# Kernel optimization log

Measured on AMD Instinct MI355X. Metric: run time of the kernel, lower is better.

## Reference

```python
import jax, jax.numpy as jnp
import numpy as np

N_NODES = 100000
N_EDGES = 1600000
IN_DIM, HID_DIM, OUT_DIM = 128, 256, 512
BN_EPS = 1e-5


def setup_inputs() -> dict:
    key = jax.random.key(0)
    ks = jax.random.split(key, 10)
    x = jax.random.normal(ks[0], (N_NODES, IN_DIM), dtype=jnp.float32)
    edge_index = jax.random.randint(ks[1], (2, N_EDGES), 0, N_NODES, dtype=jnp.int64)
    def lin(k, o, i):
        return jax.random.normal(k, (o, i), dtype=jnp.float32) * (1.0 / np.sqrt(i))
    return {
        "x": x,
        "edge_index": edge_index,
        # SAGEConv 1: in_dim -> hidden_dim (lin_l has bias, lin_r has none)
        "W1l": lin(ks[2], HID_DIM, IN_DIM),
        "b1": jnp.zeros((HID_DIM,), dtype=jnp.float32),
        "W1r": lin(ks[3], HID_DIM, IN_DIM),
        # BatchNorm1d(hidden_dim)
        "gamma": jnp.ones((HID_DIM,), dtype=jnp.float32),
        "beta": jnp.zeros((HID_DIM,), dtype=jnp.float32),
        # SAGEConv 2: hidden_dim -> gnn_out_dim
        "W2l": lin(ks[4], OUT_DIM, HID_DIM),
        "b2": jnp.zeros((OUT_DIM,), dtype=jnp.float32),
        "W2r": lin(ks[5], OUT_DIM, HID_DIM),
    }


def _sage_max(h, src, dst, Wl, b, Wr, n_nodes):
    # gather source features, max-aggregate onto destination nodes
    agg = jax.ops.segment_max(h[src], dst, num_segments=n_nodes)  # [N, D]
    agg = jnp.where(jnp.isneginf(agg), 0.0, agg)  # PyG fills empty segments with 0
    return agg @ Wl.T + b + h @ Wr.T


def reference(x, edge_index, W1l, b1, W1r, gamma, beta, W2l, b2, W2r):
    src, dst = edge_index[0], edge_index[1]
    n = x.shape[0]
    # layer 1: SAGEConv(in_dim, hidden_dim, aggr='max')
    h = _sage_max(x, src, dst, W1l, b1, W1r, n)
    # BatchNorm1d (batch statistics), Dropout is identity in eval; no activation in 'sage' branch
    mean = jnp.mean(h, axis=0)
    var = jnp.var(h, axis=0)
    h = gamma * (h - mean) * jax.lax.rsqrt(var + BN_EPS) + beta
    # layer 2: SAGEConv(hidden_dim, gnn_out_dim, aggr='max')
    out = _sage_max(h, src, dst, W2l, b2, W2r, n)
    return out
```

## Files before the change

kernel.cpp:

```cpp
#include <hip/hip_runtime.h>
#include <hip/hip_bf16.h>
#include <stdint.h>

#define N_NODES 100000
#define N_EDGES 1600000
#define IN_DIM 128
#define HID_DIM 256
#define OUT_DIM 512
#define NBUK 391
#define BCAP 8192
#define EPB 4096

typedef __attribute__((ext_vector_type(4))) float f32x4;
typedef __attribute__((ext_vector_type(8))) short bf16x8;

__device__ __forceinline__ float bf16lo(uint32_t u){ uint32_t b = u << 16; return __builtin_bit_cast(float, b); }
__device__ __forceinline__ float bf16hi(uint32_t u){ uint32_t b = u & 0xffff0000u; return __builtin_bit_cast(float, b); }
__device__ __forceinline__ uint16_t f32_to_bf16(float f){
  uint32_t u = __builtin_bit_cast(uint32_t, f);
  uint32_t r = (u + 0x7fffu + ((u >> 16) & 1u)) >> 16;
  return (uint16_t)r;
}
__device__ __forceinline__ uint32_t pack_bf16_exact(float lo, float hi){
  return (__builtin_bit_cast(uint32_t, hi) & 0xffff0000u) | (__builtin_bit_cast(uint32_t, lo) >> 16);
}
__device__ __forceinline__ uint32_t pack_bf16_rne(float lo, float hi){
  return (uint32_t)f32_to_bf16(lo) | ((uint32_t)f32_to_bf16(hi) << 16);
}
__device__ __forceinline__ void gl2lds16(const void* g, void* l){
  __builtin_amdgcn_global_load_lds(
      (const __attribute__((address_space(1))) uint32_t*)g,
      (__attribute__((address_space(3))) uint32_t*)l, 16, 0, 0);
}

__global__ void k_convx(const float* __restrict__ x, uint16_t* __restrict__ X1x,
                        int* __restrict__ gcur, float* __restrict__ sum,
                        float* __restrict__ sumsq){
  if (blockIdx.x == 12500){
    const int t = threadIdx.x;
    for (int i = t; i < NBUK; i += 256) gcur[i] = i << 13;
    sum[t] = 0.f; sumsq[t] = 0.f;
    return;
  }
  const int idx = blockIdx.x * 256 + threadIdx.x;
  const int n = idx >> 5, q = idx & 31;
  const float4 v = *(const float4*)(x + (long)n * 128 + q * 4);
  ushort4 o;
  o.x = f32_to_bf16(v.x); o.y = f32_to_bf16(v.y);
  o.z = f32_to_bf16(v.z); o.w = f32_to_bf16(v.w);
  *(ushort4*)(X1x + (long)n * 128 + q * 4) = o;
}

__global__ void k_bucket(const int* __restrict__ src, const int* __restrict__ dst,
                         int* __restrict__ gcur, int* __restrict__ ebuk){
  __shared__ int hist[NBUK], curs[NBUK], base[NBUK];
  const int tid = threadIdx.x;
  const int e0 = blockIdx.x * EPB;
  for (int t = tid; t < NBUK; t += 256) hist[t] = 0;
  __syncthreads();
  for (int i = 0; i < EPB; i += 256){
    int e = e0 + i + tid;
    if (e < N_EDGES) atomicAdd(&hist[dst[e] >> 8], 1);
  }
  __syncthreads();
  for (int t = tid; t < NBUK; t += 256){
    int h = hist[t];
    base[t] = h ? atomicAdd(&gcur[t], h) : 0;
    curs[t] = 0;
  }
  __syncthreads();
  for (int i = 0; i < EPB; i += 256){
    int e = e0 + i + tid;
    if (e < N_EDGES){
      int d = dst[e];
      int b = d >> 8;
      int idx = atomicAdd(&curs[b], 1);
      int pos = base[b] + idx;
      if (pos < ((b + 1) << 13))
        ebuk[pos] = ((d & 255) << 17) | src[e];
    }
  }
}

__global__ __launch_bounds__(256)
void k_fillc(const int* __restrict__ gcur, const int* __restrict__ ebuk,
             int* __restrict__ row_start, int* __restrict__ esrc){
  __shared__ int ebuf[BCAP];
  __shared__ int cnt[256];
  __shared__ int wtot[4];
  __shared__ int red[4];
  const int b = blockIdx.x, tid = threadIdx.x, lane = tid & 63, wv = tid >> 6;
  const int nodebase = b << 8;
  const int nodecnt = min(256, N_NODES - nodebase);
  int accb = 0;
  for (int t = tid; t < b; t += 256) accb += gcur[t] - (t << 13);
  #pragma unroll
  for (int d = 32; d > 0; d >>= 1) accb += __shfl_xor(accb, d);
  if (lane == 0) red[wv] = accb;
  int size_b = gcur[b] - (b << 13);
  if (size_b > BCAP) size_b = BCAP;
  cnt[tid] = 0;
  for (int i = tid; i < size_b; i += 256) ebuf[i] = ebuk[(b << 13) + i];
  __syncthreads();
  const int bs = red[0] + red[1] + red[2] + red[3];
  for (int i = tid; i < size_b; i += 256) atomicAdd(&cnt[ebuf[i] >> 17], 1);
  __syncthreads();
  const int c = cnt[tid];
  int v = c;
  #pragma unroll
  for (int d = 1; d < 64; d <<= 1){ int t = __shfl_up(v, d); if (lane >= d) v += t; }
  if (lane == 63) wtot[wv] = v;
  __syncthreads();
  if (tid < 4){
    int t = wtot[tid];
    #pragma unroll
    for (int d = 1; d < 4; d <<= 1){ int u = __shfl_up(t, d); if (tid >= d) t += u; }
    wtot[tid] = t;
  }
  __syncthreads();
  const int excl = (wv ? wtot[wv - 1] : 0) + (v - c);
  if (tid < nodecnt) row_start[nodebase + tid] = bs + excl;
  if (b == NBUK - 1 && tid == 0) row_start[N_NODES] = N_EDGES;
  cnt[tid] = excl;
  __syncthreads();
  for (int i = tid; i < size_b; i += 256){
    int p = ebuf[i];
    int pos = atomicAdd(&cnt[p >> 17], 1);
    esrc[bs + pos] = p & 0x1FFFF;
  }
}

__global__ void k_w1(const float* __restrict__ W1l, const float* __restrict__ W1r,
                     uint16_t* __restrict__ W1cat){
  int idx = blockIdx.x * 256 + threadIdx.x;
  int j = idx >> 8, k = idx & 255;
  float v = (k < 128) ? W1l[j * 128 + k] : W1r[j * 128 + (k - 128)];
  W1cat[idx] = f32_to_bf16(v);
}

__global__ void k_w2(const float* __restrict__ W2l, const float* __restrict__ W2r,
                     const float* __restrict__ b2, const float* __restrict__ sum,
                     const float* __restrict__ sumsq, const float* __restrict__ gamma,
                     const float* __restrict__ beta, uint16_t* __restrict__ W2cat,
                     float* __restrict__ bias2, float* __restrict__ scale_g,
                     float* __restrict__ shift_g){
  __shared__ float sc_s[256], sh_s[256];
  const int tid = threadIdx.x;
  {
    const float inv_n = 1.0f / (float)N_NODES;
    float mean = sum[tid] * inv_n;
    float var = sumsq[tid] * inv_n - mean * mean;
    float sc = gamma[tid] * rsqrtf(var + 1e-5f);
    float sh = beta[tid] - mean * sc;
    sc_s[tid] = sc; sh_s[tid] = sh;
    if (blockIdx.x == 0){ scale_g[tid] = sc; shift_g[tid] = sh; }
  }
  __syncthreads();
  const int wid = (blockIdx.x * 256 + tid) >> 6;
  const int lane = tid & 63;
  float part = 0.f;
  #pragma unroll
  for (int t = 0; t < 4; t++){
    int k = t * 64 + lane;
    float wl = W2l[(long)wid * 256 + k];
    W2cat[(long)wid * 512 + k] = f32_to_bf16(wl);
    float wr = W2r[(long)wid * 256 + k];
    W2cat[(long)wid * 512 + 256 + k] = f32_to_bf16(wr * sc_s[k]);
    part += sh_s[k] * wr;
  }
  #pragma unroll
  for (int d = 32; d > 0; d >>= 1) part += __shfl_xor(part, d);
  if (lane == 0) bias2[wid] = b2[wid] + part;
}

__global__ void k_agg1(const uint32_t* __restrict__ X1x, const int* __restrict__ row_start,
                       const int* __restrict__ esrc, uint32_t* __restrict__ X1agg){
  const int wid = (blockIdx.x * 256 + threadIdx.x) >> 6;
  const int lane = threadIdx.x & 63;
  if (wid >= N_NODES) return;
  const int grp = lane >> 4, li = lane & 15;
  const int s0 = row_start[wid], s1 = row_start[wid + 1];
  float m[8];
  #pragma unroll
  for (int j = 0; j < 8; j++) m[j] = -INFINITY;

  #define ACC1(u)                                        \
    m[0] = fmaxf(m[0], bf16lo(u.x)); m[1] = fmaxf(m[1], bf16hi(u.x)); \
    m[2] = fmaxf(m[2], bf16lo(u.y)); m[3] = fmaxf(m[3], bf16hi(u.y)); \
    m[4] = fmaxf(m[4], bf16lo(u.z)); m[5] = fmaxf(m[5], bf16hi(u.z)); \
    m[6] = fmaxf(m[6], bf16lo(u.w)); m[7] = fmaxf(m[7], bf16hi(u.w));

  int e = s0 + grp;
  for (; e + 12 < s1; e += 16){
    const uint4 ua = *(const uint4*)(X1x + (long)esrc[e] * 64 + li * 4);
    const uint4 ub = *(const uint4*)(X1x + (long)esrc[e + 4] * 64 + li * 4);
    const uint4 uc = *(const uint4*)(X1x + (long)esrc[e + 8] * 64 + li * 4);
    const uint4 ud = *(const uint4*)(X1x + (long)esrc[e + 12] * 64 + li * 4);
    ACC1(ua); ACC1(ub); ACC1(uc); ACC1(ud);
  }
  for (; e < s1; e += 4){
    const uint4 u = *(const uint4*)(X1x + (long)esrc[e] * 64 + li * 4);
    ACC1(u);
  }
  #undef ACC1
  #pragma unroll
  for (int j = 0; j < 8; j++){
    m[j] = fmaxf(m[j], __shfl_xor(m[j], 16));
    m[j] = fmaxf(m[j], __shfl_xor(m[j], 32));
  }
  if (grp == 0){
    uint4 o;
    if (s1 == s0){ o.x = o.y = o.z = o.w = 0u; }
    else {
      o.x = pack_bf16_exact(m[0], m[1]);
      o.y = pack_bf16_exact(m[2], m[3]);
      o.z = pack_bf16_exact(m[4], m[5]);
      o.w = pack_bf16_exact(m[6], m[7]);
    }
    *(uint4*)(X1agg + (long)wid * 64 + li * 4) = o;
  }
}

__global__ void k_agg2(const uint32_t* __restrict__ X2h, const int* __restrict__ row_start,
                       const int* __restrict__ esrc, const float* __restrict__ scale,
                       const float* __restrict__ shift, uint32_t* __restrict__ X2agg){
  const int wid = (blockIdx.x * 256 + threadIdx.x) >> 6;
  const int lane = threadIdx.x & 63;
  if (wid >= N_NODES) return;
  const int half = lane >> 5, li = lane & 31;
  const int c0 = li * 8;
  const float4 sca = *(const float4*)(scale + c0);
  const float4 scb = *(const float4*)(scale + c0 + 4);
  const float4 sha = *(const float4*)(shift + c0);
  const float4 shb = *(const float4*)(shift + c0 + 4);
  const int s0 = row_start[wid], s1 = row_start[wid + 1];
  float m[8];
  #pragma unroll
  for (int j = 0; j < 8; j++) m[j] = -INFINITY;

  #define ACC8(u)                                                   \
    m[0] = fmaxf(m[0], fmaf(bf16lo(u.x), sca.x, sha.x));            \
    m[1] = fmaxf(m[1], fmaf(bf16hi(u.x), sca.y, sha.y));            \
    m[2] = fmaxf(m[2], fmaf(bf16lo(u.y), sca.z, sha.z));            \
    m[3] = fmaxf(m[3], fmaf(bf16hi(u.y), sca.w, sha.w));            \
    m[4] = fmaxf(m[4], fmaf(bf16lo(u.z), scb.x, shb.x));            \
    m[5] = fmaxf(m[5], fmaf(bf16hi(u.z), scb.y, shb.y));            \
    m[6] = fmaxf(m[6], fmaf(bf16lo(u.w), scb.z, shb.z));            \
    m[7] = fmaxf(m[7], fmaf(bf16hi(u.w), scb.w, shb.w));

  int e = s0 + half;
  for (; e + 6 < s1; e += 8){
    const uint4 ua = *(const uint4*)(X2h + (long)esrc[e] * 128 + li * 4);
    const uint4 ub = *(const uint4*)(X2h + (long)esrc[e + 2] * 128 + li * 4);
    const uint4 uc = *(const uint4*)(X2h + (long)esrc[e + 4] * 128 + li * 4);
    const uint4 ud = *(const uint4*)(X2h + (long)esrc[e + 6] * 128 + li * 4);
    ACC8(ua); ACC8(ub); ACC8(uc); ACC8(ud);
  }
  for (; e < s1; e += 2){
    const uint4 u = *(const uint4*)(X2h + (long)esrc[e] * 128 + li * 4);
    ACC8(u);
  }
  #undef ACC8
  #pragma unroll
  for (int j = 0; j < 8; j++) m[j] = fmaxf(m[j], __shfl_xor(m[j], 32));
  if (half == 0){
    uint4 o;
    if (s1 == s0){ o.x = 0u; o.y = 0u; o.z = 0u; o.w = 0u; }
    else {
      o.x = pack_bf16_rne(m[0], m[1]);
      o.y = pack_bf16_rne(m[2], m[3]);
      o.z = pack_bf16_rne(m[4], m[5]);
      o.w = pack_bf16_rne(m[6], m[7]);
    }
    *(uint4*)(X2agg + (long)wid * 128 + li * 4) = o;
  }
}

template<int KT, bool EPI1>
__global__ __launch_bounds__(256, 2)
void k_gemm(const uint16_t* __restrict__ Alo, const uint16_t* __restrict__ Ahi,
            const uint16_t* __restrict__ B, const float* __restrict__ bias,
            uint16_t* __restrict__ outb, float* __restrict__ outf,
            float* __restrict__ sum, float* __restrict__ sumsq)
{
  constexpr int NSTEPS = KT / 64;
  constexpr int HSTEPS = NSTEPS / 2;
  constexpr int NT = EPI1 ? 256 : 512;
  constexpr int NW = NT / 128;
  constexpr int WG = 782 * NW;
  constexpr int PER = (WG + 7) / 8;
  __shared__ uint8_t lds[2][32768];
  const int bid = blockIdx.x;
  const int wgid = (bid & 7) * PER + (bid >> 3);
  if (wgid >= WG) return;
  const int mblk = wgid / NW, nblk = wgid % NW;
  const int tid = threadIdx.x, lane = tid & 63, wv = tid >> 6;
  const int wvm = wv >> 1, wvn = wv & 1;

  f32x4 acc[4][4] = {};

  const int srow = wv * 32 + (lane >> 3);
  const int skb  = (lane & 7) * 16;

  const uint8_t* asrc_lo[4];
  const uint8_t* asrc_hi[4];
  const uint8_t* bsrc[4];
  #pragma unroll
  for (int i = 0; i < 4; i++){
    int row = srow + i * 8;
    int kbsw = skb ^ ((row & 7) << 4);
    long grow = (long)mblk * 128 + row;
    if (grow > N_NODES - 1) grow = N_NODES - 1;
    asrc_lo[i] = (const uint8_t*)Alo + grow * KT + kbsw;
    asrc_hi[i] = (const uint8_t*)Ahi + grow * KT + kbsw;
    bsrc[i] = (const uint8_t*)B + ((long)nblk * 128 + row) * (KT * 2) + kbsw;
  }

  #define STAGE(ks, buf)                                                     \
    _Pragma("unroll")                                                        \
    for (int i = 0; i < 4; i++)                                              \
      gl2lds16((ks) < HSTEPS ? asrc_lo[i] + (ks) * 128                       \
                             : asrc_hi[i] + ((ks) - HSTEPS) * 128,           \
               &lds[buf][(wv * 4 + i) * 1024]);                              \
    _Pragma("unroll")                                                        \
    for (int i = 0; i < 4; i++)                                              \
      gl2lds16(bsrc[i] + (ks) * 128, &lds[buf][16384 + (wv * 4 + i) * 1024]);

  STAGE(0, 0);

  #pragma unroll
  for (int ks = 0; ks < NSTEPS; ++ks){
    const int cur = ks & 1;
    if (ks + 1 < NSTEPS){
      STAGE(ks + 1, cur ^ 1);
      asm volatile("s_waitcnt vmcnt(8)" ::: "memory");
    } else {
      asm volatile("s_waitcnt vmcnt(0)" ::: "memory");
    }
    __builtin_amdgcn_s_barrier();
    asm volatile("" ::: "memory");

    const uint8_t* ldsA = &lds[cur][0];
    const uint8_t* ldsB = &lds[cur][16384];
    bf16x8 af[4][2], bfr[4][2];
    #pragma unroll
    for (int m = 0; m < 4; m++){
      int row = wvm * 64 + m * 16 + (lane & 15);
      #pragma unroll
      for (int kk = 0; kk < 2; kk++){
        int kb = kk * 64 + (lane >> 4) * 16;
        af[m][kk] = *(const bf16x8*)(ldsA + row * 128 + (kb ^ ((row & 7) << 4)));
      }
    }
    #pragma unroll
    for (int n = 0; n < 4; n++){
      int row = wvn * 64 + n * 16 + (lane & 15);
      #pragma unroll
      for (int kk = 0; kk < 2; kk++){
        int kb = kk * 64 + (lane >> 4) * 16;
        bfr[n][kk] = *(const bf16x8*)(ldsB + row * 128 + (kb ^ ((row & 7) << 4)));
      }
    }
    #pragma unroll
    for (int kk = 0; kk < 2; kk++)
      #pragma unroll
      for (int m = 0; m < 4; m++)
        #pragma unroll
        for (int n = 0; n < 4; n++)
          acc[m][n] = __builtin_amdgcn_mfma_f32_16x16x32_bf16(af[m][kk], bfr[n][kk], acc[m][n], 0, 0, 0);

    asm volatile("" ::: "memory");
    __builtin_amdgcn_s_barrier();
    asm volatile("" ::: "memory");
  }
  #undef STAGE

  const int rgrp = (lane >> 4) * 4;
  #pragma unroll
  for (int n = 0; n < 4; n++){
    const int col = nblk * 128 + wvn * 64 + n * 16 + (lane & 15);
    const float bv = bias[col];
    float s1v = 0.f, s2v = 0.f;
    #pragma unroll
    for (int m = 0; m < 4; m++){
      const int rowb = mblk * 128 + wvm * 64 + m * 16 + rgrp;
      f32x4 v = acc[m][n];
      #pragma unroll
      for (int j = 0; j < 4; j++){
        const int row = rowb + j;
        const float h = v[j] + bv;
        if (row < N_NODES){
          if (EPI1){
            outb[(long)row * NT + col] = f32_to_bf16(h);
            s1v += h; s2v += h * h;
          } else {
            __builtin_nontemporal_store(h, &outf[(long)row * NT + col]);
          }
        }
      }
    }
    if (EPI1){
      s1v += __shfl_xor(s1v, 16); s1v += __shfl_xor(s1v, 32);
      s2v += __shfl_xor(s2v, 16); s2v += __shfl_xor(s2v, 32);
      if (lane < 16){
        atomicAdd(&sum[col], s1v);
        atomicAdd(&sumsq[col], s2v);
      }
    }
  }
}

extern "C" void kernel_launch(void* const* d_in, const int* in_sizes, int n_in,
                              void* d_out, int out_size, void* d_ws, size_t ws_size,
                              hipStream_t stream){
  const float* x     = (const float*)d_in[0];
  const int*   ei    = (const int*)d_in[1];
  const float* W1l   = (const float*)d_in[2];
  const float* b1    = (const float*)d_in[3];
  const float* W1r   = (const float*)d_in[4];
  const float* gamma = (const float*)d_in[5];
  const float* beta  = (const float*)d_in[6];
  const float* W2l   = (const float*)d_in[7];
  const float* b2    = (const float*)d_in[8];
  const float* W2r   = (const float*)d_in[9];
  const int* esrc_in = ei;
  const int* edst_in = ei + N_EDGES;

  uint8_t* ws = (uint8_t*)d_ws;
  uint16_t* X1agg    = (uint16_t*)(ws + 0);
  uint16_t* X1x      = (uint16_t*)(ws + 25600000);
  uint16_t* X2agg    = (uint16_t*)(ws + 51200000);
  uint16_t* X2h      = (uint16_t*)(ws + 102400000);
  int* ebuk          = (int*)(ws + 51200000);
  int* esrc          = (int*)(ws + 153600000);
  int* row_start     = (int*)(ws + 160000000);
  int* gcur          = (int*)(ws + 160402176);
  uint16_t* W1cat    = (uint16_t*)(ws + 160800256);
  uint16_t* W2cat    = (uint16_t*)(ws + 160931328);
  float* bias2       = (float*)(ws + 161455616);
  float* sum         = (float*)(ws + 161457664);
  float* sumsq       = (float*)(ws + 161458688);
  float* scale       = (float*)(ws + 161459712);
  float* shift       = (float*)(ws + 161460736);

  hipLaunchKernelGGL(k_convx, dim3(12501), dim3(256), 0, stream, x, X1x, gcur, sum, sumsq);
  hipLaunchKernelGGL(k_bucket, dim3((N_EDGES + EPB - 1) / EPB), dim3(256), 0, stream,
                     esrc_in, edst_in, gcur, ebuk);
  hipLaunchKernelGGL(k_fillc, dim3(NBUK), dim3(256), 0, stream,
                     gcur, ebuk, row_start, esrc);

  hipLaunchKernelGGL(k_w1, dim3(256), dim3(256), 0, stream, W1l, W1r, W1cat);
  hipLaunchKernelGGL(k_agg1, dim3(25000), dim3(256), 0, stream,
                     (const uint32_t*)X1x, row_start, esrc, (uint32_t*)X1agg);

  hipLaunchKernelGGL((k_gemm<256, true>), dim3(1568), dim3(256), 0, stream,
                     X1agg, X1x, W1cat, b1, X2h, (float*)nullptr, sum, sumsq);

  hipLaunchKernelGGL(k_w2, dim3(128), dim3(256), 0, stream,
                     W2l, W2r, b2, sum, sumsq, gamma, beta, W2cat, bias2, scale, shift);

  hipLaunchKernelGGL(k_agg2, dim3(25000), dim3(256), 0, stream,
                     (const uint32_t*)X2h, row_start, esrc, scale, shift, (uint32_t*)X2agg);

  hipLaunchKernelGGL((k_gemm<512, false>), dim3(3128), dim3(256), 0, stream,
                     X2agg, X2h, W2cat, bias2, (uint16_t*)nullptr, (float*)d_out,
                     (float*)nullptr, (float*)nullptr);
}
```

Before: 396.9 us.

## Process two M tiles per GEMM workgroup with continuous pipelining; halve bucket edges per block

```diff
diff --git a/kernel.cpp b/kernel.cpp
--- a/kernel.cpp
+++ b/kernel.cpp
@@ -9,7 +9,7 @@
 #define OUT_DIM 512
 #define NBUK 391
 #define BCAP 8192
-#define EPB 4096
+#define EPB 2048
 
 typedef __attribute__((ext_vector_type(4))) float f32x4;
 typedef __attribute__((ext_vector_type(8))) short bf16x8;
@@ -276,7 +276,7 @@
   }
 }
 
-template<int KT, bool EPI1>
+template<int KT, bool EPI1, int MSUB>
 __global__ __launch_bounds__(256, 2)
 void k_gemm(const uint16_t* __restrict__ Alo, const uint16_t* __restrict__ Ahi,
             const uint16_t* __restrict__ B, const float* __restrict__ bias,
@@ -285,15 +285,16 @@
 {
   constexpr int NSTEPS = KT / 64;
   constexpr int HSTEPS = NSTEPS / 2;
+  constexpr int TOT = NSTEPS * MSUB;
   constexpr int NT = EPI1 ? 256 : 512;
   constexpr int NW = NT / 128;
-  constexpr int WG = 782 * NW;
+  constexpr int WG = (782 / MSUB) * NW;
   constexpr int PER = (WG + 7) / 8;
   __shared__ uint8_t lds[2][32768];
   const int bid = blockIdx.x;
   const int wgid = (bid & 7) * PER + (bid >> 3);
   if (wgid >= WG) return;
-  const int mblk = wgid / NW, nblk = wgid % NW;
+  const int mbase = (wgid / NW) * MSUB, nblk = wgid % NW;
   const int tid = threadIdx.x, lane = tid & 63, wv = tid >> 6;
   const int wvm = wv >> 1, wvn = wv & 1;
 
@@ -302,37 +303,50 @@
   const int srow = wv * 32 + (lane >> 3);
   const int skb  = (lane & 7) * 16;
 
-  const uint8_t* asrc_lo[4];
-  const uint8_t* asrc_hi[4];
+  const uint8_t* asrc_lo[MSUB][4];
+  const uint8_t* asrc_hi[MSUB][4];
   const uint8_t* bsrc[4];
+  #pragma unroll
+  for (int s = 0; s < MSUB; s++)
+    #pragma unroll
+    for (int i = 0; i < 4; i++){
+      int row = srow + i * 8;
+      int kbsw = skb ^ ((row & 7) << 4);
+      long grow = (long)(mbase + s) * 128 + row;
+      if (grow > N_NODES - 1) grow = N_NODES - 1;
+      asrc_lo[s][i] = (const uint8_t*)Alo + grow * KT + kbsw;
+      asrc_hi[s][i] = (const uint8_t*)Ahi + grow * KT + kbsw;
+    }
   #pragma unroll
   for (int i = 0; i < 4; i++){
     int row = srow + i * 8;
     int kbsw = skb ^ ((row & 7) << 4);
-    long grow = (long)mblk * 128 + row;
-    if (grow > N_NODES - 1) grow = N_NODES - 1;
-    asrc_lo[i] = (const uint8_t*)Alo + grow * KT + kbsw;
-    asrc_hi[i] = (const uint8_t*)Ahi + grow * KT + kbsw;
     bsrc[i] = (const uint8_t*)B + ((long)nblk * 128 + row) * (KT * 2) + kbsw;
   }
 
-  #define STAGE(ks, buf)                                                     \
-    _Pragma("unroll")                                                        \
-    for (int i = 0; i < 4; i++)                                              \
-      gl2lds16((ks) < HSTEPS ? asrc_lo[i] + (ks) * 128                       \
-                             : asrc_hi[i] + ((ks) - HSTEPS) * 128,           \
-               &lds[buf][(wv * 4 + i) * 1024]);                              \
-    _Pragma("unroll")                                                        \
-    for (int i = 0; i < 4; i++)                                              \
-      gl2lds16(bsrc[i] + (ks) * 128, &lds[buf][16384 + (wv * 4 + i) * 1024]);
+  #define STAGE(t, buf)                                                        \
+    {                                                                          \
+      const int s_ = (t) / NSTEPS;                                             \
+      const int k_ = (t) % NSTEPS;                                             \
+      _Pragma("unroll")                                                        \
+      for (int i = 0; i < 4; i++)                                              \
+        gl2lds16(k_ < HSTEPS ? asrc_lo[s_][i] + k_ * 128                       \
+                             : asrc_hi[s_][i] + (k_ - HSTEPS) * 128,           \
+                 &lds[buf][(wv * 4 + i) * 1024]);                              \
+      _Pragma("unroll")                                                        \
+      for (int i = 0; i < 4; i++)                                              \
+        gl2lds16(bsrc[i] + k_ * 128, &lds[buf][16384 + (wv * 4 + i) * 1024]);  \
+    }
 
   STAGE(0, 0);
 
-  #pragma unroll
-  for (int ks = 0; ks < NSTEPS; ++ks){
-    const int cur = ks & 1;
-    if (ks + 1 < NSTEPS){
-      STAGE(ks + 1, cur ^ 1);
+  const int rgrp = (lane >> 4) * 4;
+
+  #pragma unroll
+  for (int t = 0; t < TOT; ++t){
+    const int cur = t & 1;
+    if (t + 1 < TOT){
+      STAGE(t + 1, cur ^ 1);
       asm volatile("s_waitcnt vmcnt(8)" ::: "memory");
     } else {
       asm volatile("s_waitcnt vmcnt(0)" ::: "memory");
@@ -372,42 +386,45 @@
     asm volatile("" ::: "memory");
     __builtin_amdgcn_s_barrier();
     asm volatile("" ::: "memory");
-  }
-  #undef STAGE
-
-  const int rgrp = (lane >> 4) * 4;
-  #pragma unroll
-  for (int n = 0; n < 4; n++){
-    const int col = nblk * 128 + wvn * 64 + n * 16 + (lane & 15);
-    const float bv = bias[col];
-    float s1v = 0.f, s2v = 0.f;
-    #pragma unroll
-    for (int m = 0; m < 4; m++){
-      const int rowb = mblk * 128 + wvm * 64 + m * 16 + rgrp;
-      f32x4 v = acc[m][n];
+
+    if ((t % NSTEPS) == NSTEPS - 1){
+      const int mblk = mbase + t / NSTEPS;
       #pragma unroll
-      for (int j = 0; j < 4; j++){
-        const int row = rowb + j;
-        const float h = v[j] + bv;
-        if (row < N_NODES){
-          if (EPI1){
-            outb[(long)row * NT + col] = f32_to_bf16(h);
-            s1v += h; s2v += h * h;
-          } else {
-            __builtin_nontemporal_store(h, &outf[(long)row * NT + col]);
+      for (int n = 0; n < 4; n++){
+        const int col = nblk * 128 + wvn * 64 + n * 16 + (lane & 15);
+        const float bv = bias[col];
+        float s1v = 0.f, s2v = 0.f;
+        #pragma unroll
+        for (int m = 0; m < 4; m++){
+          const int rowb = mblk * 128 + wvm * 64 + m * 16 + rgrp;
+          f32x4 v = acc[m][n];
+          #pragma unroll
+          for (int j = 0; j < 4; j++){
+            const int row = rowb + j;
+            const float h = v[j] + bv;
+            if (row < N_NODES){
+              if (EPI1){
+                outb[(long)row * NT + col] = f32_to_bf16(h);
+                s1v += h; s2v += h * h;
+              } else {
+                __builtin_nontemporal_store(h, &outf[(long)row * NT + col]);
+              }
+            }
+          }
+          acc[m][n] = (f32x4){0.f, 0.f, 0.f, 0.f};
+        }
+        if (EPI1){
+          s1v += __shfl_xor(s1v, 16); s1v += __shfl_xor(s1v, 32);
+          s2v += __shfl_xor(s2v, 16); s2v += __shfl_xor(s2v, 32);
+          if (lane < 16){
+            atomicAdd(&sum[col], s1v);
+            atomicAdd(&sumsq[col], s2v);
           }
         }
       }
     }
-    if (EPI1){
-      s1v += __shfl_xor(s1v, 16); s1v += __shfl_xor(s1v, 32);
-      s2v += __shfl_xor(s2v, 16); s2v += __shfl_xor(s2v, 32);
-      if (lane < 16){
-        atomicAdd(&sum[col], s1v);
-        atomicAdd(&sumsq[col], s2v);
-      }
-    }
-  }
+  }
+  #undef STAGE
 }
 
 extern "C" void kernel_launch(void* const* d_in, const int* in_sizes, int n_in,
@@ -444,7 +461,7 @@
   float* shift       = (float*)(ws + 161460736);
 
   hipLaunchKernelGGL(k_convx, dim3(12501), dim3(256), 0, stream, x, X1x, gcur, sum, sumsq);
-  hipLaunchKernelGGL(k_bucket, dim3((N_EDGES + EPB - 1) / EPB), dim3(256), 0, stream,
+  hipLaunchKernelGGL(k_bucket, dim3(N_EDGES / EPB + 1), dim3(256), 0, stream,
                      esrc_in, edst_in, gcur, ebuk);
   hipLaunchKernelGGL(k_fillc, dim3(NBUK), dim3(256), 0, stream,
                      gcur, ebuk, row_start, esrc);
@@ -453,7 +470,7 @@
   hipLaunchKernelGGL(k_agg1, dim3(25000), dim3(256), 0, stream,
                      (const uint32_t*)X1x, row_start, esrc, (uint32_t*)X1agg);
 
-  hipLaunchKernelGGL((k_gemm<256, true>), dim3(1568), dim3(256), 0, stream,
+  hipLaunchKernelGGL((k_gemm<256, true, 2>), dim3(784), dim3(256), 0, stream,
                      X1agg, X1x, W1cat, b1, X2h, (float*)nullptr, sum, sumsq);
 
   hipLaunchKernelGGL(k_w2, dim3(128), dim3(256), 0, stream,
@@ -462,7 +479,7 @@
   hipLaunchKernelGGL(k_agg2, dim3(25000), dim3(256), 0, stream,
                      (const uint32_t*)X2h, row_start, esrc, scale, shift, (uint32_t*)X2agg);
 
-  hipLaunchKernelGGL((k_gemm<512, false>), dim3(3128), dim3(256), 0, stream,
+  hipLaunchKernelGGL((k_gemm<512, false, 2>), dim3(1568), dim3(256), 0, stream,
                      X2agg, X2h, W2cat, bias2, (uint16_t*)nullptr, (float*)d_out,
                      (float*)nullptr, (float*)nullptr);
 }
```

New measurement: 411.3 us. +3.6%, slower.

## Enlarge GEMM tiles to 256x256 with 512-thread blocks and halve EPB

Applied to the files above, without the earlier changes.

```diff
diff --git a/kernel.cpp b/kernel.cpp
--- a/kernel.cpp
+++ b/kernel.cpp
@@ -9,7 +9,7 @@
 #define OUT_DIM 512
 #define NBUK 391
 #define BCAP 8192
-#define EPB 4096
+#define EPB 2048
 
 typedef __attribute__((ext_vector_type(4))) float f32x4;
 typedef __attribute__((ext_vector_type(8))) short bf16x8;
@@ -277,7 +277,7 @@
 }
 
 template<int KT, bool EPI1>
-__global__ __launch_bounds__(256, 2)
+__global__ __launch_bounds__(512, 2)
 void k_gemm(const uint16_t* __restrict__ Alo, const uint16_t* __restrict__ Ahi,
             const uint16_t* __restrict__ B, const float* __restrict__ bias,
             uint16_t* __restrict__ outb, float* __restrict__ outf,
@@ -286,45 +286,50 @@
   constexpr int NSTEPS = KT / 64;
   constexpr int HSTEPS = NSTEPS / 2;
   constexpr int NT = EPI1 ? 256 : 512;
-  constexpr int NW = NT / 128;
-  constexpr int WG = 782 * NW;
+  constexpr int NW = NT / 256;
+  constexpr int MT = 391;
+  constexpr int WG = MT * NW;
   constexpr int PER = (WG + 7) / 8;
-  __shared__ uint8_t lds[2][32768];
+  __shared__ uint8_t lds[2][65536];
   const int bid = blockIdx.x;
   const int wgid = (bid & 7) * PER + (bid >> 3);
   if (wgid >= WG) return;
   const int mblk = wgid / NW, nblk = wgid % NW;
   const int tid = threadIdx.x, lane = tid & 63, wv = tid >> 6;
-  const int wvm = wv >> 1, wvn = wv & 1;
-
-  f32x4 acc[4][4] = {};
-
-  const int srow = wv * 32 + (lane >> 3);
-  const int skb  = (lane & 7) * 16;
+  const int wvm = wv >> 2, wvn = wv & 3;
+
+  f32x4 acc[8][4] = {};
+
+  const int srow = tid >> 3;
+  const int skb  = (tid & 7) * 16;
+  const int kbsw = skb ^ ((srow & 7) << 4);
 
   const uint8_t* asrc_lo[4];
   const uint8_t* asrc_hi[4];
   const uint8_t* bsrc[4];
   #pragma unroll
   for (int i = 0; i < 4; i++){
-    int row = srow + i * 8;
-    int kbsw = skb ^ ((row & 7) << 4);
-    long grow = (long)mblk * 128 + row;
+    long grow = (long)mblk * 256 + i * 64 + srow;
     if (grow > N_NODES - 1) grow = N_NODES - 1;
     asrc_lo[i] = (const uint8_t*)Alo + grow * KT + kbsw;
     asrc_hi[i] = (const uint8_t*)Ahi + grow * KT + kbsw;
-    bsrc[i] = (const uint8_t*)B + ((long)nblk * 128 + row) * (KT * 2) + kbsw;
-  }
-
-  #define STAGE(ks, buf)                                                     \
-    _Pragma("unroll")                                                        \
-    for (int i = 0; i < 4; i++)                                              \
-      gl2lds16((ks) < HSTEPS ? asrc_lo[i] + (ks) * 128                       \
-                             : asrc_hi[i] + ((ks) - HSTEPS) * 128,           \
-               &lds[buf][(wv * 4 + i) * 1024]);                              \
-    _Pragma("unroll")                                                        \
-    for (int i = 0; i < 4; i++)                                              \
-      gl2lds16(bsrc[i] + (ks) * 128, &lds[buf][16384 + (wv * 4 + i) * 1024]);
+    bsrc[i] = (const uint8_t*)B + ((long)nblk * 256 + i * 64 + srow) * (KT * 2) + kbsw;
+  }
+
+  #define STAGE(ks, buf)                                                       \
+    {                                                                          \
+      const long aoff = (ks) < HSTEPS ? (long)(ks) * 128 : -1;                 \
+      _Pragma("unroll")                                                        \
+      for (int i = 0; i < 4; i++)                                              \
+        gl2lds16((ks) < HSTEPS ? asrc_lo[i] + (long)(ks) * 128                 \
+                               : asrc_hi[i] + (long)((ks) - HSTEPS) * 128,     \
+                 &lds[buf][i * 8192 + tid * 16]);                              \
+      _Pragma("unroll")                                                        \
+      for (int i = 0; i < 4; i++)                                              \
+        gl2lds16(bsrc[i] + (long)(ks) * 128,                                   \
+                 &lds[buf][32768 + i * 8192 + tid * 16]);                      \
+      (void)aoff;                                                              \
+    }
 
   STAGE(0, 0);
 
@@ -341,33 +346,27 @@
     asm volatile("" ::: "memory");
 
     const uint8_t* ldsA = &lds[cur][0];
-    const uint8_t* ldsB = &lds[cur][16384];
-    bf16x8 af[4][2], bfr[4][2];
+    const uint8_t* ldsB = &lds[cur][32768];
     #pragma unroll
-    for (int m = 0; m < 4; m++){
-      int row = wvm * 64 + m * 16 + (lane & 15);
+    for (int kk = 0; kk < 2; kk++){
+      const int kb = kk * 64 + (lane >> 4) * 16;
+      bf16x8 af[8], bfr[4];
       #pragma unroll
-      for (int kk = 0; kk < 2; kk++){
-        int kb = kk * 64 + (lane >> 4) * 16;
-        af[m][kk] = *(const bf16x8*)(ldsA + row * 128 + (kb ^ ((row & 7) << 4)));
+      for (int m = 0; m < 8; m++){
+        int row = wvm * 128 + m * 16 + (lane & 15);
+        af[m] = *(const bf16x8*)(ldsA + row * 128 + (kb ^ ((row & 7) << 4)));
       }
-    }
-    #pragma unroll
-    for (int n = 0; n < 4; n++){
-      int row = wvn * 64 + n * 16 + (lane & 15);
       #pragma unroll
-      for (int kk = 0; kk < 2; kk++){
-        int kb = kk * 64 + (lane >> 4) * 16;
-        bfr[n][kk] = *(const bf16x8*)(ldsB + row * 128 + (kb ^ ((row & 7) << 4)));
+      for (int n = 0; n < 4; n++){
+        int row = wvn * 64 + n * 16 + (lane & 15);
+        bfr[n] = *(const bf16x8*)(ldsB + row * 128 + (kb ^ ((row & 7) << 4)));
       }
-    }
-    #pragma unroll
-    for (int kk = 0; kk < 2; kk++)
       #pragma unroll
-      for (int m = 0; m < 4; m++)
+      for (int m = 0; m < 8; m++)
         #pragma unroll
         for (int n = 0; n < 4; n++)
-          acc[m][n] = __builtin_amdgcn_mfma_f32_16x16x32_bf16(af[m][kk], bfr[n][kk], acc[m][n], 0, 0, 0);
+          acc[m][n] = __builtin_amdgcn_mfma_f32_16x16x32_bf16(af[m], bfr[n], acc[m][n], 0, 0, 0);
+    }
 
     asm volatile("" ::: "memory");
     __builtin_amdgcn_s_barrier();
@@ -378,12 +377,12 @@
   const int rgrp = (lane >> 4) * 4;
   #pragma unroll
   for (int n = 0; n < 4; n++){
-    const int col = nblk * 128 + wvn * 64 + n * 16 + (lane & 15);
+    const int col = nblk * 256 + wvn * 64 + n * 16 + (lane & 15);
     const float bv = bias[col];
     float s1v = 0.f, s2v = 0.f;
     #pragma unroll
-    for (int m = 0; m < 4; m++){
-      const int rowb = mblk * 128 + wvm * 64 + m * 16 + rgrp;
+    for (int m = 0; m < 8; m++){
+      const int rowb = mblk * 256 + wvm * 128 + m * 16 + rgrp;
       f32x4 v = acc[m][n];
       #pragma unroll
       for (int j = 0; j < 4; j++){
@@ -444,7 +443,7 @@
   float* shift       = (float*)(ws + 161460736);
 
   hipLaunchKernelGGL(k_convx, dim3(12501), dim3(256), 0, stream, x, X1x, gcur, sum, sumsq);
-  hipLaunchKernelGGL(k_bucket, dim3((N_EDGES + EPB - 1) / EPB), dim3(256), 0, stream,
+  hipLaunchKernelGGL(k_bucket, dim3(N_EDGES / EPB + 1), dim3(256), 0, stream,
                      esrc_in, edst_in, gcur, ebuk);
   hipLaunchKernelGGL(k_fillc, dim3(NBUK), dim3(256), 0, stream,
                      gcur, ebuk, row_start, esrc);
@@ -453,7 +452,7 @@
   hipLaunchKernelGGL(k_agg1, dim3(25000), dim3(256), 0, stream,
                      (const uint32_t*)X1x, row_start, esrc, (uint32_t*)X1agg);
 
-  hipLaunchKernelGGL((k_gemm<256, true>), dim3(1568), dim3(256), 0, stream,
+  hipLaunchKernelGGL((k_gemm<256, true>), dim3(392), dim3(512), 0, stream,
                      X1agg, X1x, W1cat, b1, X2h, (float*)nullptr, sum, sumsq);
 
   hipLaunchKernelGGL(k_w2, dim3(128), dim3(256), 0, stream,
@@ -462,7 +461,7 @@
   hipLaunchKernelGGL(k_agg2, dim3(25000), dim3(256), 0, stream,
                      (const uint32_t*)X2h, row_start, esrc, scale, shift, (uint32_t*)X2agg);
 
-  hipLaunchKernelGGL((k_gemm<512, false>), dim3(3128), dim3(256), 0, stream,
+  hipLaunchKernelGGL((k_gemm<512, false>), dim3(784), dim3(512), 0, stream,
                      X2agg, X2h, W2cat, bias2, (uint16_t*)nullptr, (float*)d_out,
                      (float*)nullptr, (float*)nullptr);
 }
```

After: 421.3 us. 6.1% more time.

## Deepen GEMM LDS pipeline to four 32-wide K slots with prefetch distance two

Applied to the files above, without the earlier changes.

```diff
diff --git a/kernel.cpp b/kernel.cpp
--- a/kernel.cpp
+++ b/kernel.cpp
@@ -9,7 +9,7 @@
 #define OUT_DIM 512
 #define NBUK 391
 #define BCAP 8192
-#define EPB 4096
+#define EPB 2048
 
 typedef __attribute__((ext_vector_type(4))) float f32x4;
 typedef __attribute__((ext_vector_type(8))) short bf16x8;
@@ -283,13 +283,13 @@
             uint16_t* __restrict__ outb, float* __restrict__ outf,
             float* __restrict__ sum, float* __restrict__ sumsq)
 {
-  constexpr int NSTEPS = KT / 64;
+  constexpr int NSTEPS = KT / 32;
   constexpr int HSTEPS = NSTEPS / 2;
   constexpr int NT = EPI1 ? 256 : 512;
   constexpr int NW = NT / 128;
   constexpr int WG = 782 * NW;
   constexpr int PER = (WG + 7) / 8;
-  __shared__ uint8_t lds[2][32768];
+  __shared__ uint8_t lds[4][16384];
   const int bid = blockIdx.x;
   const int wgid = (bid & 7) * PER + (bid >> 3);
   if (wgid >= WG) return;
@@ -299,41 +299,46 @@
 
   f32x4 acc[4][4] = {};
 
-  const int srow = wv * 32 + (lane >> 3);
-  const int skb  = (lane & 7) * 16;
-
-  const uint8_t* asrc_lo[4];
-  const uint8_t* asrc_hi[4];
-  const uint8_t* bsrc[4];
-  #pragma unroll
-  for (int i = 0; i < 4; i++){
-    int row = srow + i * 8;
-    int kbsw = skb ^ ((row & 7) << 4);
-    long grow = (long)mblk * 128 + row;
+  const int r0 = tid >> 2;
+  const int kbs = ((tid & 3) * 16) ^ ((r0 & 3) << 4);
+
+  const uint8_t* a_lo[2];
+  const uint8_t* a_hi[2];
+  const uint8_t* b_src[2];
+  #pragma unroll
+  for (int j = 0; j < 2; j++){
+    long grow = (long)mblk * 128 + j * 64 + r0;
     if (grow > N_NODES - 1) grow = N_NODES - 1;
-    asrc_lo[i] = (const uint8_t*)Alo + grow * KT + kbsw;
-    asrc_hi[i] = (const uint8_t*)Ahi + grow * KT + kbsw;
-    bsrc[i] = (const uint8_t*)B + ((long)nblk * 128 + row) * (KT * 2) + kbsw;
-  }
-
-  #define STAGE(ks, buf)                                                     \
-    _Pragma("unroll")                                                        \
-    for (int i = 0; i < 4; i++)                                              \
-      gl2lds16((ks) < HSTEPS ? asrc_lo[i] + (ks) * 128                       \
-                             : asrc_hi[i] + ((ks) - HSTEPS) * 128,           \
-               &lds[buf][(wv * 4 + i) * 1024]);                              \
-    _Pragma("unroll")                                                        \
-    for (int i = 0; i < 4; i++)                                              \
-      gl2lds16(bsrc[i] + (ks) * 128, &lds[buf][16384 + (wv * 4 + i) * 1024]);
+    a_lo[j] = (const uint8_t*)Alo + grow * KT + kbs;
+    a_hi[j] = (const uint8_t*)Ahi + grow * KT + kbs;
+    b_src[j] = (const uint8_t*)B + ((long)nblk * 128 + j * 64 + r0) * (KT * 2) + kbs;
+  }
+
+  #define STAGE(ks, slot)                                                      \
+    {                                                                          \
+      const long aoff = (ks) < HSTEPS ? (long)(ks) * 64 : (long)((ks) - HSTEPS) * 64; \
+      const bool lo_ = (ks) < HSTEPS;                                          \
+      _Pragma("unroll")                                                        \
+      for (int j = 0; j < 2; j++)                                              \
+        gl2lds16((lo_ ? a_lo[j] : a_hi[j]) + aoff,                             \
+                 &lds[slot][j * 4096 + wv * 1024]);                            \
+      _Pragma("unroll")                                                        \
+      for (int j = 0; j < 2; j++)                                              \
+        gl2lds16(b_src[j] + (long)(ks) * 64,                                   \
+                 &lds[slot][8192 + j * 4096 + wv * 1024]);                     \
+    }
 
   STAGE(0, 0);
+  STAGE(1, 1);
 
   #pragma unroll
   for (int ks = 0; ks < NSTEPS; ++ks){
-    const int cur = ks & 1;
-    if (ks + 1 < NSTEPS){
-      STAGE(ks + 1, cur ^ 1);
+    const int cur = ks & 3;
+    if (ks + 2 < NSTEPS){
+      STAGE(ks + 2, (ks + 2) & 3);
       asm volatile("s_waitcnt vmcnt(8)" ::: "memory");
+    } else if (ks + 2 == NSTEPS){
+      asm volatile("s_waitcnt vmcnt(4)" ::: "memory");
     } else {
       asm volatile("s_waitcnt vmcnt(0)" ::: "memory");
     }
@@ -341,33 +346,24 @@
     asm volatile("" ::: "memory");
 
     const uint8_t* ldsA = &lds[cur][0];
-    const uint8_t* ldsB = &lds[cur][16384];
-    bf16x8 af[4][2], bfr[4][2];
+    const uint8_t* ldsB = &lds[cur][8192];
+    const int kb = (lane >> 4) * 16;
+    bf16x8 af[4], bfr[4];
     #pragma unroll
     for (int m = 0; m < 4; m++){
       int row = wvm * 64 + m * 16 + (lane & 15);
-      #pragma unroll
-      for (int kk = 0; kk < 2; kk++){
-        int kb = kk * 64 + (lane >> 4) * 16;
-        af[m][kk] = *(const bf16x8*)(ldsA + row * 128 + (kb ^ ((row & 7) << 4)));
-      }
+      af[m] = *(const bf16x8*)(ldsA + row * 64 + (kb ^ ((row & 3) << 4)));
     }
     #pragma unroll
     for (int n = 0; n < 4; n++){
       int row = wvn * 64 + n * 16 + (lane & 15);
+      bfr[n] = *(const bf16x8*)(ldsB + row * 64 + (kb ^ ((row & 3) << 4)));
+    }
+    #pragma unroll
+    for (int m = 0; m < 4; m++)
       #pragma unroll
-      for (int kk = 0; kk < 2; kk++){
-        int kb = kk * 64 + (lane >> 4) * 16;
-        bfr[n][kk] = *(const bf16x8*)(ldsB + row * 128 + (kb ^ ((row & 7) << 4)));
-      }
-    }
-    #pragma unroll
-    for (int kk = 0; kk < 2; kk++)
-      #pragma unroll
-      for (int m = 0; m < 4; m++)
-        #pragma unroll
-        for (int n = 0; n < 4; n++)
-          acc[m][n] = __builtin_amdgcn_mfma_f32_16x16x32_bf16(af[m][kk], bfr[n][kk], acc[m][n], 0, 0, 0);
+      for (int n = 0; n < 4; n++)
+        acc[m][n] = __builtin_amdgcn_mfma_f32_16x16x32_bf16(af[m], bfr[n], acc[m][n], 0, 0, 0);
 
     asm volatile("" ::: "memory");
     __builtin_amdgcn_s_barrier();
@@ -444,7 +440,7 @@
   float* shift       = (float*)(ws + 161460736);
 
   hipLaunchKernelGGL(k_convx, dim3(12501), dim3(256), 0, stream, x, X1x, gcur, sum, sumsq);
-  hipLaunchKernelGGL(k_bucket, dim3((N_EDGES + EPB - 1) / EPB), dim3(256), 0, stream,
+  hipLaunchKernelGGL(k_bucket, dim3(N_EDGES / EPB + 1), dim3(256), 0, stream,
                      esrc_in, edst_in, gcur, ebuk);
   hipLaunchKernelGGL(k_fillc, dim3(NBUK), dim3(256), 0, stream,
                      gcur, ebuk, row_start, esrc);
```

After: 411.0 us. 3.5% more time.
